# Performance work log

Hardware: AMD Instinct MI355X
Metric: run time of the kernel (lower is better)

The kernel has to match this reference:

```python
import jax, jax.numpy as jnp
import numpy as np

C = 256
B, H, W = 2, 64, 64


def conv1x1(x, Wt, b):
    # x: [B, Cin, H, W], Wt: [Cout, Cin], b: [Cout]
    return jnp.einsum('bchw,oc->bohw', x, Wt) + b[None, :, None, None]


def setup_inputs() -> dict:
    key = jax.random.key(0)
    ks = jax.random.split(key, 16)
    s = 0.02
    d = {
        'input1': jax.random.normal(ks[0], (B, C, H, W), jnp.float32),
        'input2': jax.random.normal(ks[1], (B, C, H, W), jnp.float32),
        'Wq1': jax.random.normal(ks[2], (C // 4, C), jnp.float32) * s,
        'bq1': jnp.zeros((C // 4,), jnp.float32),
        'Wk1': jax.random.normal(ks[3], (C // 2, C), jnp.float32) * s,
        'bk1': jnp.zeros((C // 2,), jnp.float32),
        'Wv1': jax.random.normal(ks[4], (C, C), jnp.float32) * s,
        'bv1': jnp.zeros((C,), jnp.float32),
        'Wq2': jax.random.normal(ks[5], (C // 4, C), jnp.float32) * s,
        'bq2': jnp.zeros((C // 4,), jnp.float32),
        'Wk2': jax.random.normal(ks[6], (C // 2, C), jnp.float32) * s,
        'bk2': jnp.zeros((C // 2,), jnp.float32),
        'Wv2': jax.random.normal(ks[7], (C, C), jnp.float32) * s,
        'bv2': jnp.zeros((C,), jnp.float32),
        'gamma': jax.random.normal(ks[8], (1,), jnp.float32) * 0.1,
    }
    return d


def reference(input1, input2, Wq1, bq1, Wk1, bk1, Wv1, bv1,
              Wq2, bq2, Wk2, bk2, Wv2, bv2, gamma):
    b, c, h, w = input1.shape
    hw = h * w
    q1 = conv1x1(input1, Wq1, bq1)                      # [B, C/4, H, W]
    k1 = conv1x1(input1, Wk1, bk1).reshape(b, -1, hw)   # [B, C/2, HW]
    v1 = conv1x1(input1, Wv1, bv1).reshape(b, -1, hw)   # [B, C,   HW]
    q2 = conv1x1(input2, Wq2, bq2)
    k2 = conv1x1(input2, Wk2, bk2).reshape(b, -1, hw)
    v2 = conv1x1(input2, Wv2, bv2).reshape(b, -1, hw)

    # cat on new dim 2 then 'b c t h w -> b (c t) h w' interleaves q1/q2 channels
    q = jnp.stack([q1, q2], axis=2).reshape(b, c // 2, hw)  # [B, C/2, HW]
    q = q.transpose(0, 2, 1)                                # [B, HW, C/2]

    a1 = jax.nn.softmax(jnp.einsum('bnc,bcm->bnm', q, k1), axis=-1)  # [B, HW, HW]
    out1 = jnp.einsum('bcm,bnm->bcn', v1, a1).reshape(b, c, h, w)
    out1 = gamma[0] * out1 + input1

    a2 = jax.nn.softmax(jnp.einsum('bnc,bcm->bnm', q, k2), axis=-1)
    out2 = jnp.einsum('bcm,bnm->bcn', v2, a2).reshape(b, c, h, w)
    out2 = gamma[0] * out2 + input2
    return (out1, out2)
```

## Files before the change

### kernel.cpp

```cpp
#include <hip/hip_runtime.h>

typedef __attribute__((ext_vector_type(8)))  short bf16x8;
typedef __attribute__((ext_vector_type(4)))  float f32x4;
typedef __attribute__((ext_vector_type(16))) float f32x16;
typedef __attribute__((ext_vector_type(8)))  unsigned short u16x8;

#define HW 4096
#define CDIM 256

#if __has_builtin(__builtin_amdgcn_exp2f)
#define EXP2(x) __builtin_amdgcn_exp2f(x)
#else
#define EXP2(x) exp2f(x)
#endif

__device__ __forceinline__ unsigned short f2bf(float f) {
    union { float f; unsigned u; } v; v.f = f;
    unsigned r = v.u + 0x7fffu + ((v.u >> 16) & 1u);
    return (unsigned short)(r >> 16);
}
__device__ __forceinline__ float bf2f(unsigned short u) {
    union { unsigned u; float f; } v; v.u = ((unsigned)u) << 16;
    return v.f;
}
__device__ __forceinline__ unsigned pk2(float hi, float lo) {
    union { float f; unsigned u; } a, b; a.f = hi; b.f = lo;
    return __builtin_amdgcn_perm(a.u, b.u, 0x07060302u);
}
__device__ __forceinline__ void gl_lds16(const void* g, void* l) {
    __builtin_amdgcn_global_load_lds(
        (const __attribute__((address_space(1))) unsigned int*)(unsigned long long)g,
        (__attribute__((address_space(3))) unsigned int*)(unsigned int)(unsigned long long)l,
        16, 0, 0);
}

__global__ __launch_bounds__(256) void wpack_kernel(
    const float* __restrict__ Wq1, const float* __restrict__ Wk1,
    const float* __restrict__ Wv1, const float* __restrict__ Wq2,
    const float* __restrict__ Wk2, const float* __restrict__ Wv2,
    unsigned short* __restrict__ Wpk)
{
    const int i  = blockIdx.x * 256 + threadIdx.x;
    const int c4 = i & 63;
    const int r6 = i >> 6;
    const int inp = r6 / 448;
    const int o   = r6 - inp * 448;
    const float* src;
    int orow;
    if (o < 64)       { src = inp ? Wq2 : Wq1; orow = o; }
    else if (o < 192) { src = inp ? Wk2 : Wk1; orow = o - 64; }
    else              { src = inp ? Wv2 : Wv1; orow = o - 192; }
    const float4 v = *(const float4*)(src + (size_t)orow * CDIM + c4 * 4);
    uint2 pkd; pkd.x = pk2(v.y, v.x); pkd.y = pk2(v.w, v.z);
    ((uint2*)Wpk)[i] = pkd;
}

__global__ __launch_bounds__(256) void proj_kernel(
    const float* __restrict__ in1, const float* __restrict__ in2,
    const float* __restrict__ bq1, const float* __restrict__ bk1,
    const float* __restrict__ bv1, const float* __restrict__ bq2,
    const float* __restrict__ bk2, const float* __restrict__ bv2,
    const unsigned short* __restrict__ Wpk,
    unsigned short* __restrict__ Qg, unsigned short* __restrict__ Kg,
    unsigned short* __restrict__ Vg)
{
    __shared__ unsigned xb[32 * 128];

    const int bid   = blockIdx.x;
    const int ntile = bid & 127;
    const int inp   = (bid >> 7) & 1;
    const int b     = bid >> 8;

    const float* X  = (inp ? in2 : in1) + (size_t)b * CDIM * HW;
    const float* bq = inp ? bq2 : bq1;
    const float* bk = inp ? bk2 : bk1;
    const float* bv = inp ? bv2 : bv1;
    const unsigned short* Wb = Wpk + (size_t)inp * 448 * CDIM;

    const int tid  = threadIdx.x;
    const int lane = tid & 63;
    const int w    = tid >> 6;
    const int l15  = lane & 15, quad = lane >> 4;
    const int n0   = ntile * 32;

#pragma unroll
    for (int t = 0; t < 4; ++t) {
        const int idx = t * 256 + tid;
        const int cp  = idx >> 3;
        const int n4  = idx & 7;
        const float* p0 = X + (size_t)(cp * 2) * HW + n0 + n4 * 4;
        const float4 a = *(const float4*)p0;
        const float4 bb = *(const float4*)(p0 + HW);
        const float av[4] = {a.x, a.y, a.z, a.w};
        const float bv4[4] = {bb.x, bb.y, bb.z, bb.w};
#pragma unroll
        for (int r = 0; r < 4; ++r) {
            const int n = n4 * 4 + r;
            xb[n * 128 + (((cp >> 2) ^ (n & 7)) << 2) + (cp & 3)] = pk2(bv4[r], av[r]);
        }
    }
    __syncthreads();

    f32x4 acc[7][2];
#pragma unroll
    for (int i = 0; i < 7; ++i)
#pragma unroll
        for (int j = 0; j < 2; ++j) acc[i][j] = (f32x4){0.f, 0.f, 0.f, 0.f};

#pragma unroll
    for (int kk = 0; kk < 8; ++kk) {
        bf16x8 xf[2];
#pragma unroll
        for (int ns = 0; ns < 2; ++ns) {
            const int nrow = ns * 16 + l15;
            xf[ns] = *(const bf16x8*)&xb[nrow * 128 + (((kk * 4 + quad) ^ (nrow & 7)) << 2)];
        }
#pragma unroll
        for (int os = 0; os < 7; ++os) {
            const int ob = w * 7 + os;
            const int og = ob * 16 + l15;
            const bf16x8 wf = *(const bf16x8*)(Wb + (size_t)og * CDIM + kk * 32 + quad * 8);
            if (ob < 12) {
#pragma unroll
                for (int ns = 0; ns < 2; ++ns)
                    acc[os][ns] = __builtin_amdgcn_mfma_f32_16x16x32_bf16(xf[ns], wf, acc[os][ns], 0, 0, 0);
            } else {
#pragma unroll
                for (int ns = 0; ns < 2; ++ns)
                    acc[os][ns] = __builtin_amdgcn_mfma_f32_16x16x32_bf16(wf, xf[ns], acc[os][ns], 0, 0, 0);
            }
        }
    }

    const size_t qbase = (size_t)b * HW * 128;
    const size_t kbase = (size_t)(b * 2 + inp) * HW * 128;
    const size_t vbase = (size_t)(b * 2 + inp) * (size_t)CDIM * HW;
#pragma unroll
    for (int os = 0; os < 7; ++os) {
        const int ob = w * 7 + os;
        if (ob < 4) {
            const int o = ob * 16 + l15;
            const float bb = bq[o];
#pragma unroll
            for (int ns = 0; ns < 2; ++ns) {
                const f32x4 d = acc[os][ns];
#pragma unroll
                for (int r = 0; r < 4; ++r) {
                    const int n = n0 + ns * 16 + quad * 4 + r;
                    Qg[qbase + (size_t)n * 128 + 2 * o + inp] =
                        f2bf((d[r] + bb) * 1.4426950408889634f);
                }
            }
        } else if (ob < 12) {
            const int c = (ob - 4) * 16 + l15;
            const float bb = bk[c];
#pragma unroll
            for (int ns = 0; ns < 2; ++ns) {
                const f32x4 d = acc[os][ns];
#pragma unroll
                for (int r = 0; r < 4; ++r) {
                    const int n = n0 + ns * 16 + quad * 4 + r;
                    Kg[kbase + (size_t)n * 128 + c] = f2bf(d[r] + bb);
                }
            }
        } else {
            const int c0 = (ob - 12) * 16 + quad * 4;
#pragma unroll
            for (int ns = 0; ns < 2; ++ns) {
                const f32x4 d = acc[os][ns];
#pragma unroll
                for (int r = 0; r < 4; ++r) {
                    const int n = n0 + ns * 16 + l15;
                    Vg[vbase + (size_t)(c0 + r) * HW + n] = f2bf(d[r] + bv[c0 + r]);
                }
            }
        }
    }
}

__global__ __launch_bounds__(512, 2) void attn_kernel(
    const unsigned short* __restrict__ Qg, const unsigned short* __restrict__ Kg,
    const unsigned short* __restrict__ Vg,
    unsigned short* __restrict__ Op, float* __restrict__ Lp)
{
    __shared__ __align__(16) char smem[131072];
    unsigned short* kbuf = (unsigned short*)smem;
    unsigned short* vbuf = (unsigned short*)(smem + 32768);
    unsigned*       ex32 = (unsigned*)smem;
    float*          lred = (float*)(smem + 65536);

    const int bid = blockIdx.x;
    const int mh  = bid & 1;
    const int set = (bid >> 1) & 3;
    const int att = set & 1, b = set >> 1;
    const int nt  = bid >> 3;
    const int n0g = nt * 128;
    const int mbase = mh * 2048;
    const int tid = threadIdx.x;
    const int lane = tid & 63, w = tid >> 6;
    const int nw = w & 3, mw = w >> 2;
    const int l31 = lane & 31, h = lane >> 5;

    const unsigned short* Qb = Qg + (size_t)b * HW * 128;
    const unsigned short* Kb = Kg + (size_t)(b * 2 + att) * HW * 128;
    const unsigned short* Vb = Vg + (size_t)(b * 2 + att) * (size_t)CDIM * HW;

    bf16x8 aQ[8];
    {
        const int n = n0g + nw * 32 + l31;
#pragma unroll
        for (int kk = 0; kk < 8; ++kk)
            aQ[kk] = *(const bf16x8*)(Qb + (size_t)n * 128 + kk * 16 + h * 8);
    }

    f32x16 acc[8];
#pragma unroll
    for (int i = 0; i < 8; ++i)
#pragma unroll
        for (int r = 0; r < 16; ++r) acc[i][r] = 0.f;
    float lsum = 0.f;

    const unsigned short* ksrc[2];
    const unsigned short* vsrc[4];
#pragma unroll
    for (int t = 0; t < 2; ++t) {
        const int L = t * 512 + tid;
        const int ml = L >> 4, s = L & 15;
        ksrc[t] = Kb + (size_t)ml * 128 + (s ^ (ml & 15)) * 8;
    }
#pragma unroll
    for (int t = 0; t < 4; ++t) {
        const int L = t * 512 + tid;
        const int half = L >> 10, L1 = L & 1023;
        const int c = L1 >> 2, s = L1 & 3;
        vsrc[t] = Vb + (size_t)c * HW + half * 32 + (s ^ ((c >> 2) & 3)) * 8;
    }

    auto stage = [&](int mt) {
        const int kb = mt & 1;
        const int vb = mt % 3;
        const int m0 = mbase + mt * 64;
        char* kdl = (char*)kbuf + (size_t)kb * 16384 + (size_t)w * 1024;
        char* vdl = (char*)vbuf + (size_t)vb * 32768 + (size_t)w * 1024;
#pragma unroll
        for (int t = 0; t < 2; ++t)
            gl_lds16(ksrc[t] + (size_t)m0 * 128, kdl + (size_t)t * 8192);
#pragma unroll
        for (int t = 0; t < 4; ++t)
            gl_lds16(vsrc[t] + m0, vdl + (size_t)t * 8192);
    };

    auto QK = [&](int cur, f32x16& sa, f32x16& sb) {
        const unsigned short* kb_ = kbuf + cur * 8192 + mw * 4096;
#pragma unroll
        for (int r = 0; r < 16; ++r) { sa[r] = 0.f; sb[r] = 0.f; }
#pragma unroll
        for (int kk = 0; kk < 4; ++kk) {
            bf16x8 bK = *(const bf16x8*)&kb_[(l31 * 16 + ((kk * 2 + h) ^ (l31 & 15))) * 8];
            sa = __builtin_amdgcn_mfma_f32_32x32x16_bf16(bK, aQ[kk], sa, 0, 0, 0);
        }
#pragma unroll
        for (int kk = 4; kk < 8; ++kk) {
            bf16x8 bK = *(const bf16x8*)&kb_[(l31 * 16 + ((kk * 2 + h) ^ (l31 & 15))) * 8];
            sb = __builtin_amdgcn_mfma_f32_32x32x16_bf16(bK, aQ[kk], sb, 0, 0, 0);
        }
    };

    auto EXPP = [&](const f32x16& sa, const f32x16& sb, bf16x8* bP) {
        float p[16];
#pragma unroll
        for (int r = 0; r < 16; ++r) {
            p[r] = EXP2(sa[r] + sb[r]);
            lsum += p[r];
        }
#pragma unroll
        for (int k2 = 0; k2 < 2; ++k2) {
            const float* pp = p + k2 * 8;
            const unsigned a0 = pk2(pp[1], pp[0]);
            const unsigned a1 = pk2(pp[3], pp[2]);
            const unsigned b0 = pk2(pp[5], pp[4]);
            const unsigned b1 = pk2(pp[7], pp[6]);
            auto s0 = __builtin_amdgcn_permlane32_swap(a0, b0, false, false);
            auto s1 = __builtin_amdgcn_permlane32_swap(a1, b1, false, false);
            union { unsigned u[4]; bf16x8 v; } uu;
            uu.u[0] = s0[0];
            uu.u[1] = s1[0];
            uu.u[2] = s0[1];
            uu.u[3] = s1[1];
            bP[k2] = uu.v;
        }
    };

    auto PV = [&](int vprev, const bf16x8* bP) {
        const unsigned short* vb_ = vbuf + vprev * 16384 + mw * 8192;
#pragma unroll
        for (int cf = 0; cf < 8; ++cf) {
            const int c = cf * 32 + l31;
#pragma unroll
            for (int k2 = 0; k2 < 2; ++k2) {
                bf16x8 aV = *(const bf16x8*)&vb_[(c * 4 + ((k2 * 2 + h) ^ ((c >> 2) & 3))) * 8];
                acc[cf] = __builtin_amdgcn_mfma_f32_32x32x16_bf16(aV, bP[k2], acc[cf], 0, 0, 0);
            }
        }
    };

    stage(0);
    __syncthreads();
    stage(1);
    bf16x8 bP[2];
    {
        f32x16 sa, sb;
        QK(0, sa, sb);
        EXPP(sa, sb, bP);
    }
    int vprev = 0;
#pragma unroll 1
    for (int mt = 1; mt < 32; ++mt) {
        __syncthreads();
        if (mt + 1 < 32) stage(mt + 1);
        f32x16 sa, sb;
        QK(mt & 1, sa, sb);
        PV(vprev, bP);
        EXPP(sa, sb, bP);
        vprev = (vprev == 2) ? 0 : vprev + 1;
    }
    PV(vprev, bP);

    const float lw = lsum + __shfl_xor(lsum, 32, 64);
    __syncthreads();
    if (h == 0) lred[w * 32 + l31] = lw;
    if (mw == 1) {
#pragma unroll
        for (int cf = 0; cf < 8; ++cf)
#pragma unroll
            for (int rp = 0; rp < 8; ++rp) {
                const unsigned v = ((unsigned)f2bf(acc[cf][rp * 2 + 1]) << 16)
                                 | f2bf(acc[cf][rp * 2]);
                ex32[(((w - 4) * 8 + cf) * 8 + rp) * 64 + lane] = v;
            }
    }
    __syncthreads();
    if (mw == 0) {
#pragma unroll
        for (int cf = 0; cf < 8; ++cf)
#pragma unroll
            for (int rp = 0; rp < 8; ++rp) {
                const unsigned v = ex32[((w * 8 + cf) * 8 + rp) * 64 + lane];
                acc[cf][rp * 2]     += bf2f((unsigned short)(v & 0xffffu));
                acc[cf][rp * 2 + 1] += bf2f((unsigned short)(v >> 16));
            }
        const float ltot = lred[w * 32 + l31] + lred[(w + 4) * 32 + l31];
        const int nn = n0g + nw * 32 + l31;
        if (h == 0) Lp[(size_t)(mh * 4 + set) * HW + nn] = ltot;

        const size_t obase = (size_t)(mh * 4 + set) * CDIM * HW;
#pragma unroll
        for (int cf = 0; cf < 8; ++cf) {
#pragma unroll
            for (int r = 0; r < 16; ++r) {
                const int c = cf * 32 + (r & 3) + 8 * (r >> 2) + 4 * h;
                Op[obase + (size_t)c * HW + nn] = f2bf(acc[cf][r]);
            }
        }
    }
}

__global__ __launch_bounds__(256) void combine_kernel(
    const unsigned short* __restrict__ Op, const float* __restrict__ Lp,
    const float* __restrict__ in1, const float* __restrict__ in2,
    const float* __restrict__ gamma_p, float* __restrict__ out)
{
    const size_t i8 = ((size_t)blockIdx.x * 256 + threadIdx.x) * 8;
    const int oset = (int)(i8 >> 20);
    const int att = oset >> 1, b = oset & 1;
    const int pset = b * 2 + att;
    const size_t rem = i8 & 1048575u;
    const int n = (int)(i8 & 4095);

    const u16x8 o0 = *(const u16x8*)(Op + ((size_t)pset << 20) + rem);
    const u16x8 o1 = *(const u16x8*)(Op + ((size_t)pset << 20) + rem + ((size_t)4 << 20));
    const f32x4 la0 = *(const f32x4*)(Lp + (size_t)pset * HW + n);
    const f32x4 la1 = *(const f32x4*)(Lp + (size_t)pset * HW + n + 4);
    const f32x4 lb0 = *(const f32x4*)(Lp + (size_t)(4 + pset) * HW + n);
    const f32x4 lb1 = *(const f32x4*)(Lp + (size_t)(4 + pset) * HW + n + 4);
    const float* inb = (att ? in2 : in1) + (size_t)b * CDIM * HW + rem;
    const float g = *gamma_p;

    const f32x4 iv0 = *(const f32x4*)(inb);
    const f32x4 iv1 = *(const f32x4*)(inb + 4);
    f32x4 r0, r1;
#pragma unroll
    for (int j = 0; j < 4; ++j) {
        const float ov = bf2f((unsigned short)o0[j]) + bf2f((unsigned short)o1[j]);
        r0[j] = g * ov / (la0[j] + lb0[j]) + iv0[j];
    }
#pragma unroll
    for (int j = 0; j < 4; ++j) {
        const float ov = bf2f((unsigned short)o0[j + 4]) + bf2f((unsigned short)o1[j + 4]);
        r1[j] = g * ov / (la1[j] + lb1[j]) + iv1[j];
    }
    *(f32x4*)(out + i8) = r0;
    *(f32x4*)(out + i8 + 4) = r1;
}

extern "C" void kernel_launch(void* const* d_in, const int* in_sizes, int n_in,
                              void* d_out, int out_size, void* d_ws, size_t ws_size,
                              hipStream_t stream) {
    const float* in1 = (const float*)d_in[0];
    const float* in2 = (const float*)d_in[1];
    const float* Wq1 = (const float*)d_in[2];  const float* bq1 = (const float*)d_in[3];
    const float* Wk1 = (const float*)d_in[4];  const float* bk1 = (const float*)d_in[5];
    const float* Wv1 = (const float*)d_in[6];  const float* bv1 = (const float*)d_in[7];
    const float* Wq2 = (const float*)d_in[8];  const float* bq2 = (const float*)d_in[9];
    const float* Wk2 = (const float*)d_in[10]; const float* bk2 = (const float*)d_in[11];
    const float* Wv2 = (const float*)d_in[12]; const float* bv2 = (const float*)d_in[13];
    const float* gamma = (const float*)d_in[14];

    unsigned short* Qg = (unsigned short*)d_ws;
    unsigned short* Kg = Qg + (size_t)2 * HW * 128;
    unsigned short* Vg = Kg + (size_t)4 * HW * 128;
    unsigned short* Op = Vg + (size_t)4 * CDIM * HW;
    float*          Lp = (float*)(Op + (size_t)8 * CDIM * HW);
    unsigned short* Wpk = Op;

    wpack_kernel<<<224, 256, 0, stream>>>(Wq1, Wk1, Wv1, Wq2, Wk2, Wv2, Wpk);
    proj_kernel<<<512, 256, 0, stream>>>(in1, in2, bq1, bk1, bv1, bq2, bk2, bv2,
                                         Wpk, Qg, Kg, Vg);
    attn_kernel<<<256, 512, 0, stream>>>(Qg, Kg, Vg, Op, Lp);
    combine_kernel<<<2048, 256, 0, stream>>>(Op, Lp, in1, in2, gamma, (float*)d_out);
}
```

Baseline: 177.2 us.

## Fuse softmax normalization and residual combine into attention kernel epilogue

The separate combine kernel is removed. The attention kernel now normalizes by the row sum, applies gamma and the residual, and writes the final fp32 output directly. This avoids the bf16 partial-output and row-sum round trip through global memory and one kernel launch. To make this possible the key range is no longer split across two blocks: each 256-thread block covers 64 query rows, and its two wave groups each process half of the keys before reducing through LDS. The cost is half as many waves per CU and a longer serial loop per block, which may reduce latency hiding.

```diff
diff --git a/kernel.cpp b/kernel.cpp
--- a/kernel.cpp
+++ b/kernel.cpp
@@ -178,10 +178,11 @@
     }
 }
 
-__global__ __launch_bounds__(512, 2) void attn_kernel(
+__global__ __launch_bounds__(256, 1) void attn_kernel(
     const unsigned short* __restrict__ Qg, const unsigned short* __restrict__ Kg,
     const unsigned short* __restrict__ Vg,
-    unsigned short* __restrict__ Op, float* __restrict__ Lp)
+    const float* __restrict__ in1, const float* __restrict__ in2,
+    const float* __restrict__ gamma_p, float* __restrict__ out)
 {
     __shared__ __align__(16) char smem[131072];
     unsigned short* kbuf = (unsigned short*)smem;
@@ -190,15 +191,13 @@
     float*          lred = (float*)(smem + 65536);
 
     const int bid = blockIdx.x;
-    const int mh  = bid & 1;
-    const int set = (bid >> 1) & 3;
+    const int set = bid & 3;
     const int att = set & 1, b = set >> 1;
-    const int nt  = bid >> 3;
-    const int n0g = nt * 128;
-    const int mbase = mh * 2048;
+    const int nt  = bid >> 2;
+    const int n0g = nt * 64;
     const int tid = threadIdx.x;
     const int lane = tid & 63, w = tid >> 6;
-    const int nw = w & 3, mw = w >> 2;
+    const int nw = w & 1, mw = w >> 1;
     const int l31 = lane & 31, h = lane >> 5;
 
     const unsigned short* Qb = Qg + (size_t)b * HW * 128;
@@ -220,34 +219,34 @@
         for (int r = 0; r < 16; ++r) acc[i][r] = 0.f;
     float lsum = 0.f;
 
-    const unsigned short* ksrc[2];
-    const unsigned short* vsrc[4];
-#pragma unroll
-    for (int t = 0; t < 2; ++t) {
-        const int L = t * 512 + tid;
-        const int ml = L >> 4, s = L & 15;
-        ksrc[t] = Kb + (size_t)ml * 128 + (s ^ (ml & 15)) * 8;
-    }
+    const unsigned short* ksrc[4];
+    const unsigned short* vsrc[8];
 #pragma unroll
     for (int t = 0; t < 4; ++t) {
-        const int L = t * 512 + tid;
+        const int L = t * 256 + tid;
+        const int half = L >> 9, Lh = L & 511;
+        const int ml = Lh >> 4, s = Lh & 15;
+        ksrc[t] = Kb + (size_t)(half * 2048 + ml) * 128 + (s ^ (ml & 15)) * 8;
+    }
+#pragma unroll
+    for (int t = 0; t < 8; ++t) {
+        const int L = t * 256 + tid;
         const int half = L >> 10, L1 = L & 1023;
         const int c = L1 >> 2, s = L1 & 3;
-        vsrc[t] = Vb + (size_t)c * HW + half * 32 + (s ^ ((c >> 2) & 3)) * 8;
+        vsrc[t] = Vb + (size_t)c * HW + half * 2048 + (s ^ ((c >> 2) & 3)) * 8;
     }
 
     auto stage = [&](int mt) {
-        const int kb = mt & 1;
-        const int vb = mt % 3;
-        const int m0 = mbase + mt * 64;
-        char* kdl = (char*)kbuf + (size_t)kb * 16384 + (size_t)w * 1024;
-        char* vdl = (char*)vbuf + (size_t)vb * 32768 + (size_t)w * 1024;
-#pragma unroll
-        for (int t = 0; t < 2; ++t)
-            gl_lds16(ksrc[t] + (size_t)m0 * 128, kdl + (size_t)t * 8192);
+        const int kb = mt & 1, vb = mt % 3;
+        const int m0 = mt * 32;
+        char* kdl = smem + (size_t)kb * 16384 + (size_t)w * 1024;
+        char* vdl = smem + 32768 + (size_t)vb * 32768 + (size_t)w * 1024;
 #pragma unroll
         for (int t = 0; t < 4; ++t)
-            gl_lds16(vsrc[t] + m0, vdl + (size_t)t * 8192);
+            gl_lds16(ksrc[t] + (size_t)m0 * 128, kdl + (size_t)t * 4096);
+#pragma unroll
+        for (int t = 0; t < 8; ++t)
+            gl_lds16(vsrc[t] + m0, vdl + (size_t)t * 4096);
     };
 
     auto QK = [&](int cur, f32x16& sa, f32x16& sb) {
@@ -315,9 +314,9 @@
     }
     int vprev = 0;
 #pragma unroll 1
-    for (int mt = 1; mt < 32; ++mt) {
+    for (int mt = 1; mt < 64; ++mt) {
         __syncthreads();
-        if (mt + 1 < 32) stage(mt + 1);
+        if (mt + 1 < 64) stage(mt + 1);
         f32x16 sa, sb;
         QK(mt & 1, sa, sb);
         PV(vprev, bP);
@@ -336,71 +335,31 @@
             for (int rp = 0; rp < 8; ++rp) {
                 const unsigned v = ((unsigned)f2bf(acc[cf][rp * 2 + 1]) << 16)
                                  | f2bf(acc[cf][rp * 2]);
-                ex32[(((w - 4) * 8 + cf) * 8 + rp) * 64 + lane] = v;
+                ex32[(nw * 64 + cf * 8 + rp) * 64 + lane] = v;
             }
     }
     __syncthreads();
     if (mw == 0) {
-#pragma unroll
-        for (int cf = 0; cf < 8; ++cf)
+        const float g = *gamma_p;
+        const int nn = n0g + nw * 32 + l31;
+        const float ltot = lred[w * 32 + l31] + lred[(w + 2) * 32 + l31];
+        const float* inb = (att ? in2 : in1) + (size_t)b * CDIM * HW;
+        float* outb = out + (size_t)(att * 2 + b) * CDIM * HW;
+#pragma unroll
+        for (int cf = 0; cf < 8; ++cf) {
 #pragma unroll
             for (int rp = 0; rp < 8; ++rp) {
-                const unsigned v = ex32[((w * 8 + cf) * 8 + rp) * 64 + lane];
-                acc[cf][rp * 2]     += bf2f((unsigned short)(v & 0xffffu));
-                acc[cf][rp * 2 + 1] += bf2f((unsigned short)(v >> 16));
-            }
-        const float ltot = lred[w * 32 + l31] + lred[(w + 4) * 32 + l31];
-        const int nn = n0g + nw * 32 + l31;
-        if (h == 0) Lp[(size_t)(mh * 4 + set) * HW + nn] = ltot;
-
-        const size_t obase = (size_t)(mh * 4 + set) * CDIM * HW;
-#pragma unroll
-        for (int cf = 0; cf < 8; ++cf) {
-#pragma unroll
-            for (int r = 0; r < 16; ++r) {
-                const int c = cf * 32 + (r & 3) + 8 * (r >> 2) + 4 * h;
-                Op[obase + (size_t)c * HW + nn] = f2bf(acc[cf][r]);
-            }
-        }
-    }
-}
-
-__global__ __launch_bounds__(256) void combine_kernel(
-    const unsigned short* __restrict__ Op, const float* __restrict__ Lp,
-    const float* __restrict__ in1, const float* __restrict__ in2,
-    const float* __restrict__ gamma_p, float* __restrict__ out)
-{
-    const size_t i8 = ((size_t)blockIdx.x * 256 + threadIdx.x) * 8;
-    const int oset = (int)(i8 >> 20);
-    const int att = oset >> 1, b = oset & 1;
-    const int pset = b * 2 + att;
-    const size_t rem = i8 & 1048575u;
-    const int n = (int)(i8 & 4095);
-
-    const u16x8 o0 = *(const u16x8*)(Op + ((size_t)pset << 20) + rem);
-    const u16x8 o1 = *(const u16x8*)(Op + ((size_t)pset << 20) + rem + ((size_t)4 << 20));
-    const f32x4 la0 = *(const f32x4*)(Lp + (size_t)pset * HW + n);
-    const f32x4 la1 = *(const f32x4*)(Lp + (size_t)pset * HW + n + 4);
-    const f32x4 lb0 = *(const f32x4*)(Lp + (size_t)(4 + pset) * HW + n);
-    const f32x4 lb1 = *(const f32x4*)(Lp + (size_t)(4 + pset) * HW + n + 4);
-    const float* inb = (att ? in2 : in1) + (size_t)b * CDIM * HW + rem;
-    const float g = *gamma_p;
-
-    const f32x4 iv0 = *(const f32x4*)(inb);
-    const f32x4 iv1 = *(const f32x4*)(inb + 4);
-    f32x4 r0, r1;
-#pragma unroll
-    for (int j = 0; j < 4; ++j) {
-        const float ov = bf2f((unsigned short)o0[j]) + bf2f((unsigned short)o1[j]);
-        r0[j] = g * ov / (la0[j] + lb0[j]) + iv0[j];
-    }
-#pragma unroll
-    for (int j = 0; j < 4; ++j) {
-        const float ov = bf2f((unsigned short)o0[j + 4]) + bf2f((unsigned short)o1[j + 4]);
-        r1[j] = g * ov / (la1[j] + lb1[j]) + iv1[j];
-    }
-    *(f32x4*)(out + i8) = r0;
-    *(f32x4*)(out + i8 + 4) = r1;
+                const unsigned v = ex32[(nw * 64 + cf * 8 + rp) * 64 + lane];
+                const float o0 = acc[cf][rp * 2]     + bf2f((unsigned short)(v & 0xffffu));
+                const float o1 = acc[cf][rp * 2 + 1] + bf2f((unsigned short)(v >> 16));
+                const int r0i = rp * 2, r1i = rp * 2 + 1;
+                const int c0 = cf * 32 + (r0i & 3) + 8 * (r0i >> 2) + 4 * h;
+                const int c1 = cf * 32 + (r1i & 3) + 8 * (r1i >> 2) + 4 * h;
+                outb[(size_t)c0 * HW + nn] = g * o0 / ltot + inb[(size_t)c0 * HW + nn];
+                outb[(size_t)c1 * HW + nn] = g * o1 / ltot + inb[(size_t)c1 * HW + nn];
+            }
+        }
+    }
 }
 
 extern "C" void kernel_launch(void* const* d_in, const int* in_sizes, int n_in,
@@ -419,13 +378,10 @@
     unsigned short* Qg = (unsigned short*)d_ws;
     unsigned short* Kg = Qg + (size_t)2 * HW * 128;
     unsigned short* Vg = Kg + (size_t)4 * HW * 128;
-    unsigned short* Op = Vg + (size_t)4 * CDIM * HW;
-    float*          Lp = (float*)(Op + (size_t)8 * CDIM * HW);
-    unsigned short* Wpk = Op;
+    unsigned short* Wpk = Vg + (size_t)4 * CDIM * HW;
 
     wpack_kernel<<<224, 256, 0, stream>>>(Wq1, Wk1, Wv1, Wq2, Wk2, Wv2, Wpk);
     proj_kernel<<<512, 256, 0, stream>>>(in1, in2, bq1, bk1, bv1, bq2, bk2, bv2,
                                          Wpk, Qg, Kg, Vg);
-    attn_kernel<<<256, 512, 0, stream>>>(Qg, Kg, Vg, Op, Lp);
-    combine_kernel<<<2048, 256, 0, stream>>>(Op, Lp, in1, in2, gamma, (float*)d_out);
-}
+    attn_kernel<<<256, 256, 0, stream>>>(Qg, Kg, Vg, in1, in2, gamma, (float*)d_out);
+}
```

New measurement: 208.8 us. 1.18x slower.
